# Optimization experiments

Hardware: AMD Instinct MI355X
Metric: run time of the kernel (lower is better)

The kernel has to match this reference:

```python
import jax, jax.numpy as jnp
import numpy as np

T, D, H = 2048, 1024, 16
HS = D // H  # head_size = 64
DFF = 4 * D
LN_EPS = 1e-6


def layernorm(x, scale, bias, eps=LN_EPS):
    mu = jnp.mean(x, axis=-1, keepdims=True)
    var = jnp.mean(jnp.square(x - mu), axis=-1, keepdims=True)
    return (x - mu) * jax.lax.rsqrt(var + eps) * scale + bias


def setup_inputs() -> dict:
    key = jax.random.key(0)
    ks = jax.random.split(key, 12)
    s_in = 1.0 / np.sqrt(D)
    s_ff = 1.0 / np.sqrt(DFF)
    return {
        "x": jax.random.normal(ks[0], (T, D), jnp.float32),
        "Wq": jax.random.normal(ks[1], (H, D, HS), jnp.float32) * s_in,
        "Wk": jax.random.normal(ks[2], (H, D, HS), jnp.float32) * s_in,
        "Wv": jax.random.normal(ks[3], (H, D, HS), jnp.float32) * s_in,
        "Wo": jax.random.normal(ks[4], (D, D), jnp.float32) * s_in,
        "bo": jnp.zeros((D,), jnp.float32),
        "W1": jax.random.normal(ks[5], (D, DFF), jnp.float32) * s_in,
        "b1": jnp.zeros((DFF,), jnp.float32),
        "W2": jax.random.normal(ks[6], (DFF, D), jnp.float32) * s_ff,
        "b2": jnp.zeros((D,), jnp.float32),
        "ln1_scale": jnp.ones((D,), jnp.float32),
        "ln1_bias": jnp.zeros((D,), jnp.float32),
        "ln2_scale": jnp.ones((D,), jnp.float32),
        "ln2_bias": jnp.zeros((D,), jnp.float32),
        "training": 0,
    }


def reference(x, Wq, Wk, Wv, Wo, bo, W1, b1, W2, b2,
              ln1_scale, ln1_bias, ln2_scale, ln2_bias, training):
    # --- pre-LN causal multi-head self-attention ---
    h = layernorm(x, ln1_scale, ln1_bias)
    q = jnp.einsum("td,hdk->htk", h, Wq)  # [H,T,HS]
    k = jnp.einsum("td,hdk->htk", h, Wk)
    v = jnp.einsum("td,hdk->htk", h, Wv)
    scores = jnp.einsum("htk,hsk->hts", q, k) / jnp.sqrt(jnp.float32(HS))
    causal = jnp.tril(jnp.ones((T, T), jnp.float32))
    scores = jnp.where(causal == 0, -jnp.inf, scores)
    wei = jax.nn.softmax(scores, axis=-1)
    av = jnp.einsum("hts,hsk->htk", wei, v)          # [H,T,HS]
    av = av.transpose(1, 0, 2).reshape(T, H * HS)    # concat over heads
    x = x + av @ Wo + bo                              # dropout deterministic -> identity
    # --- pre-LN feed-forward ---
    h2 = layernorm(x, ln2_scale, ln2_bias)
    ff = jax.nn.relu(h2 @ W1 + b1) @ W2 + b2
    x = x + ff
    return x
```

## Files before the change

kernel.cpp:

```cpp
#include <hip/hip_runtime.h>
#include <cstdint>


typedef __bf16 bf16;
typedef __bf16 bf16x4 __attribute__((ext_vector_type(4)));
typedef __bf16 bf16x8 __attribute__((ext_vector_type(8)));
typedef float floatx4 __attribute__((ext_vector_type(4)));

__device__ __forceinline__ void ld_g2l(const bf16* g, bf16* l) {
    __builtin_amdgcn_global_load_lds(
        (const __attribute__((address_space(1))) void*)g,
        (__attribute__((address_space(3))) void*)l, 16, 0, 0);
}

__device__ __forceinline__ void ln_row_body(
    const float* __restrict__ x, const float* __restrict__ sc,
    const float* __restrict__ bi, bf16* __restrict__ out,
    int row, int tid, float* wred)
{
    const float4 v = ((const float4*)(x + (size_t)row * 1024))[tid];
    float s1 = v.x + v.y + v.z + v.w;
    float s2 = v.x * v.x + v.y * v.y + v.z * v.z + v.w * v.w;
#pragma unroll
    for (int mm = 1; mm < 64; mm <<= 1) {
        s1 += __shfl_xor(s1, mm);
        s2 += __shfl_xor(s2, mm);
    }
    const int wave = tid >> 6, lane = tid & 63;
    if (lane == 0) { wred[wave] = s1; wred[4 + wave] = s2; }
    __syncthreads();
    s1 = wred[0] + wred[1] + wred[2] + wred[3];
    s2 = wred[4] + wred[5] + wred[6] + wred[7];
    const float mu = s1 * (1.f / 1024.f);
    const float var = fmaxf(s2 * (1.f / 1024.f) - mu * mu, 0.f);
    const float rr = rsqrtf(var + 1e-6f);
    const float4 scv = ((const float4*)sc)[tid];
    const float4 biv = ((const float4*)bi)[tid];
    bf16x4 ov;
    ov[0] = (bf16)((v.x - mu) * rr * scv.x + biv.x);
    ov[1] = (bf16)((v.y - mu) * rr * scv.y + biv.y);
    ov[2] = (bf16)((v.z - mu) * rr * scv.z + biv.z);
    ov[3] = (bf16)((v.w - mu) * rr * scv.w + biv.w);
    *(bf16x4*)(out + (size_t)row * 1024 + tid * 4) = ov;
}

__global__ __launch_bounds__(256) void prep_kernel(
    const float* __restrict__ Wq, const float* __restrict__ Wk,
    const float* __restrict__ Wv, bf16* __restrict__ Wqkvt,
    const float* __restrict__ Wo, bf16* __restrict__ Wot,
    const float* __restrict__ W1, bf16* __restrict__ W1t,
    const float* __restrict__ W2, bf16* __restrict__ W2t,
    const float* __restrict__ x, const float* __restrict__ ln1s,
    const float* __restrict__ ln1b, bf16* __restrict__ hbuf)
{
    __shared__ float tile[32][33];
    __shared__ float wred[8];
    const int b = blockIdx.x;
    const int tid = threadIdx.x;

    if (b >= 12288) {
        ln_row_body(x, ln1s, ln1b, hbuf, b - 12288, tid, wred);
        return;
    }

    const int tx = tid & 31, ty = tid >> 5;
    const float* src; bf16* dst; int R, C, c0, r0;
    if (b < 3072) {
        const int bz = b >> 6, by = (b >> 1) & 31, bx = b & 1;
        const int m = bz >> 4, h = bz & 15;
        src = (m == 0 ? Wq : (m == 1 ? Wk : Wv)) + h * 65536;
        dst = Wqkvt + m * 1048576 + h * 65536;
        R = 1024; C = 64; c0 = bx * 32; r0 = by * 32;
    } else if (b < 4096) {
        const int i = b - 3072;
        src = Wo; dst = Wot; R = 1024; C = 1024;
        c0 = (i & 31) * 32; r0 = (i >> 5) * 32;
    } else if (b < 8192) {
        const int i = b - 4096;
        src = W1; dst = W1t; R = 1024; C = 4096;
        c0 = (i & 127) * 32; r0 = (i >> 7) * 32;
    } else {
        const int i = b - 8192;
        src = W2; dst = W2t; R = 4096; C = 1024;
        c0 = (i & 31) * 32; r0 = (i >> 5) * 32;
    }
#pragma unroll
    for (int i = ty; i < 32; i += 8)
        tile[i][tx] = src[(size_t)(r0 + i) * C + c0 + tx];
    __syncthreads();
#pragma unroll
    for (int i = ty; i < 32; i += 8)
        dst[(size_t)(c0 + i) * R + r0 + tx] = (bf16)tile[tx][i];
}

__global__ __launch_bounds__(256) void ln_kernel(
    const float* __restrict__ x, const float* __restrict__ sc,
    const float* __restrict__ bi, bf16* __restrict__ out)
{
    __shared__ float wred[8];
    ln_row_body(x, sc, bi, out, blockIdx.x, threadIdx.x, wred);
}

__global__ __launch_bounds__(256) void transpose_head_kernel(
    const bf16* __restrict__ qkv, bf16* __restrict__ dst, int colOff)
{
    __shared__ bf16 tile[32][33];
    const int tx = threadIdx.x, ty = threadIdx.y;
    const int h = blockIdx.z;
    const int j0 = blockIdx.x * 32, s0 = blockIdx.y * 32;
#pragma unroll
    for (int i = ty; i < 32; i += 8)
        tile[i][tx] = qkv[(size_t)(s0 + i) * 3072 + colOff + h * 64 + j0 + tx];
    __syncthreads();
#pragma unroll
    for (int i = ty; i < 32; i += 8)
        dst[(size_t)h * 64 * 2048 + (size_t)(j0 + i) * 2048 + s0 + tx] = tile[tx][i];
}

__global__ __launch_bounds__(256) void reduce4_kernel(
    const float* __restrict__ p, const float* __restrict__ bias,
    const float* __restrict__ res, float* __restrict__ out)
{
    const int idx = blockIdx.x * 256 + threadIdx.x;
    const int c4 = idx & 255;
    const float4 a0 = ((const float4*)p)[idx];
    const float4 a1 = ((const float4*)(p + 2097152))[idx];
    const float4 a2 = ((const float4*)(p + 4194304))[idx];
    const float4 a3 = ((const float4*)(p + 6291456))[idx];
    const float4 bi = ((const float4*)bias)[c4];
    const float4 r = ((const float4*)res)[idx];
    float4 o;
    o.x = (a0.x + a1.x) + (a2.x + a3.x) + bi.x + r.x;
    o.y = (a0.y + a1.y) + (a2.y + a3.y) + bi.y + r.y;
    o.z = (a0.z + a1.z) + (a2.z + a3.z) + bi.z + r.z;
    o.w = (a0.w + a1.w) + (a2.w + a3.w) + bi.w + r.w;
    ((float4*)out)[idx] = o;
}

template <int MODE, int NG, int MG, int SPLITK>
__global__ __launch_bounds__(256) void gemm128_kernel(
    const bf16* __restrict__ A, const bf16* __restrict__ Bt,
    int N, int K,
    float* __restrict__ outF, bf16* __restrict__ outB,
    const float* __restrict__ bias)
{
    __shared__ __align__(16) bf16 Alds[2][128][32];
    __shared__ __align__(16) bf16 Blds[2][128][32];
    const int tid  = threadIdx.x;
    const int lane = tid & 63;
    const int w    = tid >> 6;
    const int r15  = lane & 15;
    const int quad = lane >> 4;

    const int id    = blockIdx.x + gridDim.x * (blockIdx.y + gridDim.y * blockIdx.z);
    const int xcd   = id & 7;
    const int seq   = id >> 3;
    const int nPerX = gridDim.x / NG;
    const int mPerX = gridDim.y / MG;
    const int nm    = nPerX * mPerX;
    const int z     = seq / nm;
    const int loc   = seq - z * nm;
    const int bn    = ((xcd % NG) * nPerX + (loc % nPerX)) * 128;
    const int bm    = ((xcd / NG) * mPerX + (loc / nPerX)) * 128;

    const int wm = (w >> 1) * 64;
    const int wn = (w & 1) * 64;

    floatx4 acc[4][4];
#pragma unroll
    for (int i = 0; i < 4; ++i)
#pragma unroll
        for (int j = 0; j < 4; ++j) acc[i][j] = (floatx4)(0.f);

    const int KS    = K / SPLITK;
    const int kBase = (SPLITK > 1) ? z * KS : 0;
    const int nIter = KS / 32;

    const int srow = lane >> 2;
    const int gch  = (lane & 3) ^ ((lane >> 3) & 3);
    const bf16* aptr = A + (size_t)(bm + w * 16 + srow) * K + kBase + gch * 8;
    const bf16* bptr = Bt + (size_t)(bn + w * 16 + srow) * K + kBase + gch * 8;

#pragma unroll
    for (int rr = 0; rr < 2; ++rr) {
        ld_g2l(aptr + (size_t)rr * 64 * K, &Alds[0][rr * 64 + w * 16][0]);
        ld_g2l(bptr + (size_t)rr * 64 * K, &Blds[0][rr * 64 + w * 16][0]);
    }

    const int pcs = quad ^ ((r15 >> 1) & 3);

    for (int it = 0; it < nIter; ++it) {
        const int buf = it & 1;
        __syncthreads();
        if (it + 1 < nIter) {
            const int k2 = (it + 1) * 32;
#pragma unroll
            for (int rr = 0; rr < 2; ++rr) {
                ld_g2l(aptr + (size_t)rr * 64 * K + k2, &Alds[buf ^ 1][rr * 64 + w * 16][0]);
                ld_g2l(bptr + (size_t)rr * 64 * K + k2, &Blds[buf ^ 1][rr * 64 + w * 16][0]);
            }
        }
        bf16x8 af[4], bfr[4];
#pragma unroll
        for (int i = 0; i < 4; ++i)
            af[i] = *(const bf16x8*)(&Alds[buf][wm + i * 16 + r15][pcs * 8]);
#pragma unroll
        for (int j = 0; j < 4; ++j)
            bfr[j] = *(const bf16x8*)(&Blds[buf][wn + j * 16 + r15][pcs * 8]);
#pragma unroll
        for (int i = 0; i < 4; ++i)
#pragma unroll
            for (int j = 0; j < 4; ++j)
                acc[i][j] = __builtin_amdgcn_mfma_f32_16x16x32_bf16(
                    af[i], bfr[j], acc[i][j], 0, 0, 0);
    }

    const int row0 = bm + wm + quad * 4;
    const int col0 = bn + wn + r15;
    float* po = (MODE == 3) ? outF + (size_t)z * 2048 * 1024 : outF;
#pragma unroll
    for (int i = 0; i < 4; ++i) {
#pragma unroll
        for (int reg = 0; reg < 4; ++reg) {
            const int row = row0 + i * 16 + reg;
#pragma unroll
            for (int j = 0; j < 4; ++j) {
                const int col = col0 + j * 16;
                float v = acc[i][j][reg];
                if (MODE == 0) {
                    outB[(size_t)row * N + col] = (bf16)v;
                } else if (MODE == 2) {
                    v += bias[col];
                    outB[(size_t)row * N + col] = (bf16)fmaxf(v, 0.f);
                } else {
                    po[(size_t)row * N + col] = v;
                }
            }
        }
    }
}

template <int NG, int MG>
__global__ __launch_bounds__(256) void gemm64_kernel(
    const bf16* __restrict__ A, const bf16* __restrict__ Bt,
    int N, int K,
    float* __restrict__ outF, const float* __restrict__ bias,
    const float* __restrict__ res)
{
    __shared__ __align__(16) bf16 Alds[2][64][64];
    __shared__ __align__(16) bf16 Blds[2][64][64];
    const int tid  = threadIdx.x;
    const int lane = tid & 63;
    const int w    = tid >> 6;
    const int r15  = lane & 15;
    const int quad = lane >> 4;

    const int id    = blockIdx.x + gridDim.x * blockIdx.y;
    const int xcd   = id & 7;
    const int seq   = id >> 3;
    const int nPerX = gridDim.x / NG;
    const int mPerX = gridDim.y / MG;
    const int loc   = seq % (nPerX * mPerX);
    const int bn    = ((xcd % NG) * nPerX + (loc % nPerX)) * 64;
    const int bm    = ((xcd / NG) * mPerX + (loc / nPerX)) * 64;

    const int wm = (w >> 1) * 32;
    const int wn = (w & 1) * 32;

    floatx4 acc[2][2];
#pragma unroll
    for (int i = 0; i < 2; ++i)
#pragma unroll
        for (int j = 0; j < 2; ++j) acc[i][j] = (floatx4)(0.f);

    const int nIter = K / 64;
    const int lrow = lane >> 3;
    const int gch  = (lane & 7) ^ lrow;
    const bf16* aptr = A + (size_t)(bm + w * 16 + lrow) * K + gch * 8;
    const bf16* bptr = Bt + (size_t)(bn + w * 16 + lrow) * K + gch * 8;

#pragma unroll
    for (int t = 0; t < 2; ++t) {
        ld_g2l(aptr + (size_t)t * 8 * K, &Alds[0][w * 16 + t * 8][0]);
        ld_g2l(bptr + (size_t)t * 8 * K, &Blds[0][w * 16 + t * 8][0]);
    }

    for (int it = 0; it < nIter; ++it) {
        const int buf = it & 1;
        __syncthreads();
        if (it + 1 < nIter) {
            const int k2 = (it + 1) * 64;
#pragma unroll
            for (int t = 0; t < 2; ++t) {
                ld_g2l(aptr + (size_t)t * 8 * K + k2, &Alds[buf ^ 1][w * 16 + t * 8][0]);
                ld_g2l(bptr + (size_t)t * 8 * K + k2, &Blds[buf ^ 1][w * 16 + t * 8][0]);
            }
        }
#pragma unroll
        for (int kk = 0; kk < 2; ++kk) {
            const int pc = ((kk * 4 + quad) ^ (r15 & 7)) * 8;
            bf16x8 af[2], bfr[2];
#pragma unroll
            for (int i = 0; i < 2; ++i)
                af[i] = *(const bf16x8*)(&Alds[buf][wm + i * 16 + r15][pc]);
#pragma unroll
            for (int j = 0; j < 2; ++j)
                bfr[j] = *(const bf16x8*)(&Blds[buf][wn + j * 16 + r15][pc]);
#pragma unroll
            for (int i = 0; i < 2; ++i)
#pragma unroll
                for (int j = 0; j < 2; ++j)
                    acc[i][j] = __builtin_amdgcn_mfma_f32_16x16x32_bf16(
                        af[i], bfr[j], acc[i][j], 0, 0, 0);
        }
    }

    const int row0 = bm + wm + quad * 4;
    const int col0 = bn + wn + r15;
#pragma unroll
    for (int i = 0; i < 2; ++i)
#pragma unroll
        for (int reg = 0; reg < 4; ++reg) {
            const int row = row0 + i * 16 + reg;
#pragma unroll
            for (int j = 0; j < 2; ++j) {
                const int col = col0 + j * 16;
                outF[(size_t)row * N + col] =
                    acc[i][j][reg] + bias[col] + res[(size_t)row * N + col];
            }
        }
}

__global__ __launch_bounds__(256) void attn_kernel(
    const bf16* __restrict__ qkv, const bf16* __restrict__ vt,
    bf16* __restrict__ out)
{
    __shared__ __align__(16) bf16 Qs[64][64];
    __shared__ __align__(16) bf16 Ks[2][64][64];
    __shared__ __align__(16) bf16 Vs[2][64][64];
    __shared__ __align__(16) bf16 Ps[4][16][72];

    const int tid  = threadIdx.x;
    const int w    = tid >> 6;
    const int lane = tid & 63;
    const int r15  = lane & 15;
    const int quad = lane >> 4;
    const int rl   = lane >> 3;
    const int gsw  = (lane & 7) ^ (rl & 7);

    const int idp = blockIdx.x + 16 * blockIdx.y;
    const int seq = idp >> 3;
    const int h   = (idp & 7) * 2 + (seq & 1);
    const int qp  = seq >> 1;
    const int qt  = blockIdx.z ? 31 - qp : qp;
    const int qrow0 = qt * 64;

    const bf16* qsec = qkv + h * 64;
    const bf16* ksec = qkv + 1024 + h * 64;
    const bf16* vth  = vt + (size_t)h * 64 * 2048;

#pragma unroll
    for (int t = 0; t < 2; ++t) {
        const int r = t * 32 + w * 8 + rl;
        ld_g2l(qsec + (size_t)(qrow0 + r) * 3072 + gsw * 8, &Qs[t * 32 + w * 8][0]);
        ld_g2l(ksec + (size_t)r * 3072 + gsw * 8, &Ks[0][t * 32 + w * 8][0]);
        ld_g2l(vth + (size_t)r * 2048 + gsw * 8, &Vs[0][t * 32 + w * 8][0]);
    }
    __syncthreads();

    bf16x8 qf[2];
#pragma unroll
    for (int c = 0; c < 2; ++c) {
        const int p = ((c * 4 + quad) ^ (r15 & 7)) * 8;
        qf[c] = *(const bf16x8*)&Qs[w * 16 + r15][p];
    }

    float lacc[4] = {0.f, 0.f, 0.f, 0.f};
    floatx4 O[4];
#pragma unroll
    for (int j = 0; j < 4; ++j) O[j] = (floatx4)(0.f);

#pragma unroll 1
    for (int sb = 0; sb <= qt; ++sb) {
        const int buf = sb & 1;
        if (sb < qt) {
            const int s1 = (sb + 1) * 64;
#pragma unroll
            for (int t = 0; t < 2; ++t) {
                const int r = t * 32 + w * 8 + rl;
                ld_g2l(ksec + (size_t)(s1 + r) * 3072 + gsw * 8, &Ks[buf ^ 1][t * 32 + w * 8][0]);
                ld_g2l(vth + (size_t)r * 2048 + s1 + gsw * 8, &Vs[buf ^ 1][t * 32 + w * 8][0]);
            }
        }

        floatx4 S[4];
#pragma unroll
        for (int j = 0; j < 4; ++j) S[j] = (floatx4)(0.f);
#pragma unroll
        for (int c = 0; c < 2; ++c) {
#pragma unroll
            for (int j = 0; j < 4; ++j) {
                const int p = ((c * 4 + quad) ^ (r15 & 7)) * 8;
                const bf16x8 b = *(const bf16x8*)&Ks[buf][j * 16 + r15][p];
                S[j] = __builtin_amdgcn_mfma_f32_16x16x32_bf16(qf[c], b, S[j], 0, 0, 0);
            }
        }
        const bool diag = (sb == qt);
        const int rowl = w * 16 + quad * 4;
#pragma unroll
        for (int j = 0; j < 4; ++j) {
            const int col = j * 16 + r15;
#pragma unroll
            for (int r = 0; r < 4; ++r) {
                float p = exp2f(fmaf(S[j][r], 0.18033688f, -28.853901f));
                if (diag && col > rowl + r) p = 0.f;
                S[j][r] = p;
                lacc[r] += p;
            }
        }
#pragma unroll
        for (int r = 0; r < 4; ++r)
#pragma unroll
            for (int j = 0; j < 4; ++j)
                Ps[w][quad * 4 + r][j * 16 + r15] = (bf16)S[j][r];
#pragma unroll
        for (int c = 0; c < 2; ++c) {
            const bf16x8 a = *(const bf16x8*)&Ps[w][r15][c * 32 + quad * 8];
#pragma unroll
            for (int j = 0; j < 4; ++j) {
                const int p = ((c * 4 + quad) ^ (r15 & 7)) * 8;
                const bf16x8 b = *(const bf16x8*)&Vs[buf][j * 16 + r15][p];
                O[j] = __builtin_amdgcn_mfma_f32_16x16x32_bf16(a, b, O[j], 0, 0, 0);
            }
        }
        __syncthreads();
    }
#pragma unroll
    for (int r = 0; r < 4; ++r) {
#pragma unroll
        for (int d = 1; d < 16; d <<= 1) lacc[r] += __shfl_xor(lacc[r], d);
    }
#pragma unroll
    for (int r = 0; r < 4; ++r) {
        const float inv = 1.0f / lacc[r];
        const int row = qrow0 + w * 16 + quad * 4 + r;
#pragma unroll
        for (int j = 0; j < 4; ++j)
            out[(size_t)row * 1024 + h * 64 + j * 16 + r15] = (bf16)(O[j][r] * inv);
    }
}

extern "C" void kernel_launch(void* const* d_in, const int* in_sizes, int n_in,
                              void* d_out, int out_size, void* d_ws, size_t ws_size,
                              hipStream_t stream)
{
    const float* x    = (const float*)d_in[0];
    const float* Wq   = (const float*)d_in[1];
    const float* Wk   = (const float*)d_in[2];
    const float* Wv   = (const float*)d_in[3];
    const float* Wo   = (const float*)d_in[4];
    const float* bo   = (const float*)d_in[5];
    const float* W1   = (const float*)d_in[6];
    const float* b1   = (const float*)d_in[7];
    const float* W2   = (const float*)d_in[8];
    const float* b2   = (const float*)d_in[9];
    const float* ln1s = (const float*)d_in[10];
    const float* ln1b = (const float*)d_in[11];
    const float* ln2s = (const float*)d_in[12];
    const float* ln2b = (const float*)d_in[13];

    char* ws = (char*)d_ws;
    bf16*  Wqkvt = (bf16*)(ws + 0);
    bf16*  Wot   = (bf16*)(ws + 6291456);
    bf16*  W1t   = (bf16*)(ws + 8388608);
    bf16*  W2t   = (bf16*)(ws + 16777216);
    bf16*  hbuf  = (bf16*)(ws + 25165824);
    bf16*  QKV   = (bf16*)(ws + 29360128);
    bf16*  Vt    = (bf16*)(ws + 41943040);
    bf16*  Obuf  = (bf16*)(ws + 46137344);
    float* x1    = (float*)(ws + 50331648);
    bf16*  h2    = (bf16*)(ws + 58720256);
    bf16*  ff1   = (bf16*)(ws + 62914560);
    float* psum  = (float*)(ws + 79691776);

    const dim3 tb(32, 8);

    prep_kernel<<<14336, 256, 0, stream>>>(Wq, Wk, Wv, Wqkvt, Wo, Wot,
                                           W1, W1t, W2, W2t,
                                           x, ln1s, ln1b, hbuf);
    gemm128_kernel<0,4,2,1><<<dim3(24, 16), 256, 0, stream>>>(hbuf, Wqkvt, 3072, 1024, nullptr, QKV, nullptr);
    transpose_head_kernel<<<dim3(2, 64, 16), tb, 0, stream>>>(QKV, Vt, 2048);
    attn_kernel<<<dim3(16, 16, 2), 256, 0, stream>>>(QKV, Vt, Obuf);
    gemm64_kernel<4,2><<<dim3(16, 32), 256, 0, stream>>>(Obuf, Wot, 1024, 1024, x1, bo, x);
    ln_kernel<<<2048, 256, 0, stream>>>(x1, ln2s, ln2b, h2);
    gemm128_kernel<2,4,2,1><<<dim3(32, 16), 256, 0, stream>>>(h2, W1t, 4096, 1024, nullptr, ff1, b1);
    gemm128_kernel<3,2,4,4><<<dim3(8, 16, 4), 256, 0, stream>>>(ff1, W2t, 1024, 4096, psum, nullptr, nullptr);
    reduce4_kernel<<<2048, 256, 0, stream>>>(psum, b2, x1, (float*)d_out);
}
```

Baseline: 273.7 us.

## Deepen GEMM K-tile to 64 and enlarge prep transpose tiles to 64x64

The 128x128 GEMM kernel now stages 64-wide K slices in LDS per iteration instead of 32, with a new XOR swizzle over eight 16-byte chunks and two MFMA sub-steps per tile. This halves the number of barrier-separated iterations and gives more outstanding global-to-LDS loads per sync. The weight transpose/convert prep kernel uses 64x64 tiles, so it launches far fewer blocks. LDS use per GEMM block doubles to 64 KB, which may reduce occupancy.

Result: faster. 250.9 us (-8.3%).

```diff
diff --git a/kernel.cpp b/kernel.cpp
--- a/kernel.cpp
+++ b/kernel.cpp
@@ -53,43 +53,43 @@
     const float* __restrict__ x, const float* __restrict__ ln1s,
     const float* __restrict__ ln1b, bf16* __restrict__ hbuf)
 {
-    __shared__ float tile[32][33];
+    __shared__ float tile[64][65];
     __shared__ float wred[8];
     const int b = blockIdx.x;
     const int tid = threadIdx.x;
 
-    if (b >= 12288) {
-        ln_row_body(x, ln1s, ln1b, hbuf, b - 12288, tid, wred);
+    if (b >= 3072) {
+        ln_row_body(x, ln1s, ln1b, hbuf, b - 3072, tid, wred);
         return;
     }
 
-    const int tx = tid & 31, ty = tid >> 5;
+    const int tx = tid & 63, ty = tid >> 6;
     const float* src; bf16* dst; int R, C, c0, r0;
-    if (b < 3072) {
-        const int bz = b >> 6, by = (b >> 1) & 31, bx = b & 1;
-        const int m = bz >> 4, h = bz & 15;
+    if (b < 768) {
+        const int sec = b >> 4, ti = b & 15;
+        const int m = sec >> 4, h = sec & 15;
         src = (m == 0 ? Wq : (m == 1 ? Wk : Wv)) + h * 65536;
         dst = Wqkvt + m * 1048576 + h * 65536;
-        R = 1024; C = 64; c0 = bx * 32; r0 = by * 32;
-    } else if (b < 4096) {
-        const int i = b - 3072;
+        R = 1024; C = 64; c0 = 0; r0 = ti * 64;
+    } else if (b < 1024) {
+        const int i = b - 768;
         src = Wo; dst = Wot; R = 1024; C = 1024;
-        c0 = (i & 31) * 32; r0 = (i >> 5) * 32;
-    } else if (b < 8192) {
-        const int i = b - 4096;
+        c0 = (i & 15) * 64; r0 = (i >> 4) * 64;
+    } else if (b < 2048) {
+        const int i = b - 1024;
         src = W1; dst = W1t; R = 1024; C = 4096;
-        c0 = (i & 127) * 32; r0 = (i >> 7) * 32;
+        c0 = (i & 63) * 64; r0 = (i >> 6) * 64;
     } else {
-        const int i = b - 8192;
+        const int i = b - 2048;
         src = W2; dst = W2t; R = 4096; C = 1024;
-        c0 = (i & 31) * 32; r0 = (i >> 5) * 32;
-    }
-#pragma unroll
-    for (int i = ty; i < 32; i += 8)
+        c0 = (i & 15) * 64; r0 = (i >> 4) * 64;
+    }
+#pragma unroll
+    for (int i = ty; i < 64; i += 4)
         tile[i][tx] = src[(size_t)(r0 + i) * C + c0 + tx];
     __syncthreads();
 #pragma unroll
-    for (int i = ty; i < 32; i += 8)
+    for (int i = ty; i < 64; i += 4)
         dst[(size_t)(c0 + i) * R + r0 + tx] = (bf16)tile[tx][i];
 }
 
@@ -144,8 +144,8 @@
     float* __restrict__ outF, bf16* __restrict__ outB,
     const float* __restrict__ bias)
 {
-    __shared__ __align__(16) bf16 Alds[2][128][32];
-    __shared__ __align__(16) bf16 Blds[2][128][32];
+    __shared__ __align__(16) bf16 Alds[2][128][64];
+    __shared__ __align__(16) bf16 Blds[2][128][64];
     const int tid  = threadIdx.x;
     const int lane = tid & 63;
     const int w    = tid >> 6;
@@ -174,45 +174,53 @@
 
     const int KS    = K / SPLITK;
     const int kBase = (SPLITK > 1) ? z * KS : 0;
-    const int nIter = KS / 32;
-
-    const int srow = lane >> 2;
-    const int gch  = (lane & 3) ^ ((lane >> 3) & 3);
-    const bf16* aptr = A + (size_t)(bm + w * 16 + srow) * K + kBase + gch * 8;
-    const bf16* bptr = Bt + (size_t)(bn + w * 16 + srow) * K + kBase + gch * 8;
-
-#pragma unroll
-    for (int rr = 0; rr < 2; ++rr) {
-        ld_g2l(aptr + (size_t)rr * 64 * K, &Alds[0][rr * 64 + w * 16][0]);
-        ld_g2l(bptr + (size_t)rr * 64 * K, &Blds[0][rr * 64 + w * 16][0]);
-    }
-
-    const int pcs = quad ^ ((r15 >> 1) & 3);
+    const int nIter = KS / 64;
+
+    const int lrow = lane >> 3;
+    const int gch  = (lane & 7) ^ lrow;
+    const bf16* aptr = A + (size_t)(bm + w * 16 + lrow) * K + kBase + gch * 8;
+    const bf16* bptr = Bt + (size_t)(bn + w * 16 + lrow) * K + kBase + gch * 8;
+
+#pragma unroll
+    for (int rr = 0; rr < 2; ++rr)
+#pragma unroll
+        for (int t = 0; t < 2; ++t) {
+            ld_g2l(aptr + (size_t)(rr * 64 + t * 8) * K, &Alds[0][rr * 64 + w * 16 + t * 8][0]);
+            ld_g2l(bptr + (size_t)(rr * 64 + t * 8) * K, &Blds[0][rr * 64 + w * 16 + t * 8][0]);
+        }
 
     for (int it = 0; it < nIter; ++it) {
         const int buf = it & 1;
         __syncthreads();
         if (it + 1 < nIter) {
-            const int k2 = (it + 1) * 32;
-#pragma unroll
-            for (int rr = 0; rr < 2; ++rr) {
-                ld_g2l(aptr + (size_t)rr * 64 * K + k2, &Alds[buf ^ 1][rr * 64 + w * 16][0]);
-                ld_g2l(bptr + (size_t)rr * 64 * K + k2, &Blds[buf ^ 1][rr * 64 + w * 16][0]);
-            }
-        }
-        bf16x8 af[4], bfr[4];
-#pragma unroll
-        for (int i = 0; i < 4; ++i)
-            af[i] = *(const bf16x8*)(&Alds[buf][wm + i * 16 + r15][pcs * 8]);
-#pragma unroll
-        for (int j = 0; j < 4; ++j)
-            bfr[j] = *(const bf16x8*)(&Blds[buf][wn + j * 16 + r15][pcs * 8]);
-#pragma unroll
-        for (int i = 0; i < 4; ++i)
+            const int k2 = (it + 1) * 64;
+#pragma unroll
+            for (int rr = 0; rr < 2; ++rr)
+#pragma unroll
+                for (int t = 0; t < 2; ++t) {
+                    ld_g2l(aptr + (size_t)(rr * 64 + t * 8) * K + k2,
+                           &Alds[buf ^ 1][rr * 64 + w * 16 + t * 8][0]);
+                    ld_g2l(bptr + (size_t)(rr * 64 + t * 8) * K + k2,
+                           &Blds[buf ^ 1][rr * 64 + w * 16 + t * 8][0]);
+                }
+        }
+#pragma unroll
+        for (int kk = 0; kk < 2; ++kk) {
+            const int pc = ((kk * 4 + quad) ^ (r15 & 7)) * 8;
+            bf16x8 af[4], bfr[4];
+#pragma unroll
+            for (int i = 0; i < 4; ++i)
+                af[i] = *(const bf16x8*)(&Alds[buf][wm + i * 16 + r15][pc]);
 #pragma unroll
             for (int j = 0; j < 4; ++j)
-                acc[i][j] = __builtin_amdgcn_mfma_f32_16x16x32_bf16(
-                    af[i], bfr[j], acc[i][j], 0, 0, 0);
+                bfr[j] = *(const bf16x8*)(&Blds[buf][wn + j * 16 + r15][pc]);
+#pragma unroll
+            for (int i = 0; i < 4; ++i)
+#pragma unroll
+                for (int j = 0; j < 4; ++j)
+                    acc[i][j] = __builtin_amdgcn_mfma_f32_16x16x32_bf16(
+                        af[i], bfr[j], acc[i][j], 0, 0, 0);
+        }
     }
 
     const int row0 = bm + wm + quad * 4;
@@ -485,9 +493,9 @@
 
     const dim3 tb(32, 8);
 
-    prep_kernel<<<14336, 256, 0, stream>>>(Wq, Wk, Wv, Wqkvt, Wo, Wot,
-                                           W1, W1t, W2, W2t,
-                                           x, ln1s, ln1b, hbuf);
+    prep_kernel<<<5120, 256, 0, stream>>>(Wq, Wk, Wv, Wqkvt, Wo, Wot,
+                                          W1, W1t, W2, W2t,
+                                          x, ln1s, ln1b, hbuf);
     gemm128_kernel<0,4,2,1><<<dim3(24, 16), 256, 0, stream>>>(hbuf, Wqkvt, 3072, 1024, nullptr, QKV, nullptr);
     transpose_head_kernel<<<dim3(2, 64, 16), tb, 0, stream>>>(QKV, Vt, 2048);
     attn_kernel<<<dim3(16, 16, 2), 256, 0, stream>>>(QKV, Vt, Obuf);
```
